# Kernel tuning notes

Measured on AMD Instinct MI355X. Metric: run time of the kernel, lower is better.

The kernel has to match this reference:

```python
import jax, jax.numpy as jnp
import numpy as np

INPUTS = 41024  # halfkp feature count (64 king squares * 641)
L1, L2, L3 = 128, 32, 32
B = 4096
ACTIVE_P = 30.0 / INPUTS  # ~30 active features per position


def setup_inputs() -> dict:
    key = jax.random.key(0)
    ks = jax.random.split(key, 10)
    # side-to-move indicators: us in {0,1}, them = 1 - us
    us = jax.random.randint(ks[0], (B, 1), 0, 2).astype(jnp.float32)
    them = 1.0 - us
    # sparse halfkp feature vectors (~30 active one-hot features per row)
    def sparse_feats(k):
        k1, k2 = jax.random.split(k)
        mask = jax.random.bernoulli(k1, ACTIVE_P, (B, INPUTS))
        return mask.astype(jnp.float32)
    w_in = sparse_feats(ks[1])
    b_in = sparse_feats(ks[2])
    s = 0.02
    W_ft = jax.random.normal(ks[3], (INPUTS, L1), dtype=jnp.float32) * s
    b_ft = jax.random.normal(ks[4], (L1,), dtype=jnp.float32) * s
    W1 = jax.random.normal(ks[5], (2 * L1, L2), dtype=jnp.float32) * s
    b1 = jax.random.normal(ks[6], (L2,), dtype=jnp.float32) * s
    W2 = jax.random.normal(ks[7], (L2, L3), dtype=jnp.float32) * s
    b2 = jax.random.normal(ks[8], (L3,), dtype=jnp.float32) * s
    Wo = jax.random.normal(ks[9], (L3, 1), dtype=jnp.float32) * s
    bo = jnp.zeros((1,), dtype=jnp.float32)
    return {"us": us, "them": them, "w_in": w_in, "b_in": b_in,
            "W_ft": W_ft, "b_ft": b_ft, "W1": W1, "b1": b1,
            "W2": W2, "b2": b2, "Wo": Wo, "bo": bo}


def reference(us, them, w_in, b_in, W_ft, b_ft, W1, b1, W2, b2, Wo, bo):
    # feature transformer (shared weights for white/black perspectives)
    w = w_in @ W_ft + b_ft  # [B, L1]
    b = b_in @ W_ft + b_ft  # [B, L1]
    l0 = us * jnp.concatenate([w, b], axis=1) + them * jnp.concatenate([b, w], axis=1)
    l0 = jnp.clip(l0, 0.0, 1.0)
    l1 = jnp.clip(l0 @ W1 + b1, 0.0, 1.0)
    l2 = jnp.clip(l1 @ W2 + b2, 0.0, 1.0)
    return l2 @ Wo + bo  # [B, 1]
```

## Files before the change

### kernel.cpp

```cpp
#include <hip/hip_runtime.h>
#include <hip/hip_bf16.h>

#define NNUE_INPUTS 41024
#define L1N 128
#define L2N 32
#define L3N 32
#define MAX_ACT 512

__device__ __forceinline__ float clip01(float x) {
    return fminf(fmaxf(x, 0.0f), 1.0f);
}

__global__ __launch_bounds__(256, 4) void nnue_fused_kernel(
    const float* __restrict__ us, const float* __restrict__ them,
    const float* __restrict__ w_in, const float* __restrict__ b_in,
    const float* __restrict__ W_ft, const float* __restrict__ b_ft,
    const float* __restrict__ W1, const float* __restrict__ b1,
    const float* __restrict__ W2, const float* __restrict__ b2,
    const float* __restrict__ Wo, const float* __restrict__ bo,
    float* __restrict__ out)
{
    __shared__ int   s_idx_w[MAX_ACT];
    __shared__ int   s_idx_b[MAX_ACT];
    __shared__ int   s_cnt[2];
    __shared__ float s_w[L1N];
    __shared__ float s_b[L1N];
    __shared__ float s_l0[2 * L1N];
    __shared__ float s_part[8][L2N];
    __shared__ float s_l1[L2N];
    __shared__ float s_l2[L3N];

    const int row = blockIdx.x;
    const int tid = threadIdx.x;

    if (tid < 2) s_cnt[tid] = 0;
    const float u = us[row];
    const float t = them[row];
    __syncthreads();

    const float4* wr = (const float4*)(w_in + (size_t)row * NNUE_INPUTS);
    const float4* br = (const float4*)(b_in + (size_t)row * NNUE_INPUTS);
    const int nv8 = NNUE_INPUTS / 8;

    for (int v = tid; v < nv8; v += 256) {
        const float4 a0 = wr[2 * v];
        const float4 a1 = wr[2 * v + 1];
        const float4 c0 = br[2 * v];
        const float4 c1 = br[2 * v + 1];
        const float sw = ((a0.x + a0.y) + (a0.z + a0.w)) + ((a1.x + a1.y) + (a1.z + a1.w));
        const float sb = ((c0.x + c0.y) + (c0.z + c0.w)) + ((c1.x + c1.y) + (c1.z + c1.w));
        if (__any((sw != 0.0f) || (sb != 0.0f))) {
            const int base = v * 8;
            if (sw != 0.0f) {
                unsigned m = (a0.x != 0.0f ?   1u : 0u) | (a0.y != 0.0f ?   2u : 0u)
                           | (a0.z != 0.0f ?   4u : 0u) | (a0.w != 0.0f ?   8u : 0u)
                           | (a1.x != 0.0f ?  16u : 0u) | (a1.y != 0.0f ?  32u : 0u)
                           | (a1.z != 0.0f ?  64u : 0u) | (a1.w != 0.0f ? 128u : 0u);
                while (m) {
                    const int b = __ffs(m) - 1; m &= m - 1;
                    const int p = atomicAdd(&s_cnt[0], 1);
                    s_idx_w[p & (MAX_ACT - 1)] = base + b;
                }
            }
            if (sb != 0.0f) {
                unsigned m = (c0.x != 0.0f ?   1u : 0u) | (c0.y != 0.0f ?   2u : 0u)
                           | (c0.z != 0.0f ?   4u : 0u) | (c0.w != 0.0f ?   8u : 0u)
                           | (c1.x != 0.0f ?  16u : 0u) | (c1.y != 0.0f ?  32u : 0u)
                           | (c1.z != 0.0f ?  64u : 0u) | (c1.w != 0.0f ? 128u : 0u);
                while (m) {
                    const int b = __ffs(m) - 1; m &= m - 1;
                    const int p = atomicAdd(&s_cnt[1], 1);
                    s_idx_b[p & (MAX_ACT - 1)] = base + b;
                }
            }
        }
    }
    __syncthreads();

    const int kw = min(s_cnt[0], MAX_ACT);
    const int kb = min(s_cnt[1], MAX_ACT);

    {
        const int  c    = tid & (L1N - 1);
        const bool is_b = tid >= L1N;
        const int* lst  = is_b ? s_idx_b : s_idx_w;
        const int  K    = is_b ? kb : kw;
        const float* Wc = W_ft + c;
        float acc = b_ft[c];
        int k = 0;
        for (; k + 4 <= K; k += 4) {
            const int i0 = lst[k], i1 = lst[k + 1], i2 = lst[k + 2], i3 = lst[k + 3];
            const float f0 = Wc[(size_t)i0 * L1N];
            const float f1 = Wc[(size_t)i1 * L1N];
            const float f2 = Wc[(size_t)i2 * L1N];
            const float f3 = Wc[(size_t)i3 * L1N];
            acc += f0; acc += f1; acc += f2; acc += f3;
        }
        for (; k < K; ++k) acc += Wc[(size_t)lst[k] * L1N];
        if (is_b) s_b[c] = acc; else s_w[c] = acc;
    }
    __syncthreads();

    if (tid < L1N) {
        const float wv = s_w[tid], bv = s_b[tid];
        s_l0[tid]       = clip01(u * wv + t * bv);
        s_l0[L1N + tid] = clip01(u * bv + t * wv);
    }
    __syncthreads();

    {
        const int o  = tid & 31;
        const int ch = tid >> 5;
        float a = 0.0f;
        const int k0 = ch * 32;
        #pragma unroll
        for (int k = 0; k < 32; ++k) {
            a += s_l0[k0 + k] * W1[(k0 + k) * L2N + o];
        }
        s_part[ch][o] = a;
    }
    __syncthreads();
    if (tid < L2N) {
        float a = b1[tid];
        #pragma unroll
        for (int j = 0; j < 8; ++j) a += s_part[j][tid];
        s_l1[tid] = clip01(a);
    }
    __syncthreads();

    if (tid < L3N) {
        float a = b2[tid];
        #pragma unroll
        for (int k = 0; k < L2N; ++k) a += s_l1[k] * W2[k * L3N + tid];
        s_l2[tid] = clip01(a);
    }
    __syncthreads();

    if (tid == 0) {
        float a = bo[0];
        #pragma unroll
        for (int k = 0; k < L3N; ++k) a += s_l2[k] * Wo[k];
        out[row] = a;
    }
}

extern "C" void kernel_launch(void* const* d_in, const int* in_sizes, int n_in,
                              void* d_out, int out_size, void* d_ws, size_t ws_size,
                              hipStream_t stream) {
    const float* us   = (const float*)d_in[0];
    const float* them = (const float*)d_in[1];
    const float* w_in = (const float*)d_in[2];
    const float* b_in = (const float*)d_in[3];
    const float* W_ft = (const float*)d_in[4];
    const float* b_ft = (const float*)d_in[5];
    const float* W1   = (const float*)d_in[6];
    const float* b1   = (const float*)d_in[7];
    const float* W2   = (const float*)d_in[8];
    const float* b2   = (const float*)d_in[9];
    const float* Wo   = (const float*)d_in[10];
    const float* bo   = (const float*)d_in[11];
    float* out = (float*)d_out;

    const int B = in_sizes[0];
    nnue_fused_kernel<<<dim3(B), dim3(256), 0, stream>>>(
        us, them, w_in, b_in, W_ft, b_ft, W1, b1, W2, b2, Wo, bo, out);
}
```

Baseline: 1.234 ms.

## Split sparse-input scan into a separate grid-strided kernel with global index lists

The per-row nonzero scan of the dense one-hot inputs moves into its own kernel. That kernel uses a fixed 2048-block grid that streams both input matrices flat with four independent float4 loads per iteration, and it appends active feature indices to per-row lists in workspace using global atomics. A second kernel reads those lists and does the feature-transformer gather and the small MLP. The goal is better memory-level parallelism and bandwidth on the dominant 1.3 GB streaming read. The cost is a memset, an extra launch, global atomic traffic, and index lists that are no longer in order, which changes the float summation order.

```diff
diff --git a/kernel.cpp b/kernel.cpp
--- a/kernel.cpp
+++ b/kernel.cpp
@@ -2,6 +2,7 @@
 #include <hip/hip_bf16.h>
 
 #define NNUE_INPUTS 41024
+#define NV4_ROW (NNUE_INPUTS / 4)
 #define L1N 128
 #define L2N 32
 #define L3N 32
@@ -11,18 +12,69 @@
     return fminf(fmaxf(x, 0.0f), 1.0f);
 }
 
-__global__ __launch_bounds__(256, 4) void nnue_fused_kernel(
+__global__ __launch_bounds__(256, 8) void nnue_scan_kernel(
+    const float* __restrict__ w_in, const float* __restrict__ b_in,
+    int* __restrict__ cnt,
+    int* __restrict__ idx,
+    int rows)
+{
+    const int  half = gridDim.x >> 1;
+    const int  p    = (blockIdx.x >= half) ? 1 : 0;
+    const int  blk  = p ? (blockIdx.x - half) : blockIdx.x;
+    const float4* src = (const float4*)(p ? b_in : w_in);
+    int* mycnt = cnt + (size_t)p * rows;
+    int* myidx = idx + (size_t)p * rows * MAX_ACT;
+
+    const long NV4    = (long)rows * NV4_ROW;
+    const long tcount = (long)half * 256;
+
+    auto put = [&](int e) {
+        const int r  = (unsigned)e / NNUE_INPUTS;
+        const int f  = e - r * NNUE_INPUTS;
+        const int pp = atomicAdd(&mycnt[r], 1);
+        myidx[(size_t)r * MAX_ACT + (pp & (MAX_ACT - 1))] = f;
+    };
+    auto emit = [&](const float4& x, long v) {
+        const float s = (x.x + x.y) + (x.z + x.w);
+        if (s != 0.0f) {
+            const int e = (int)(v * 4);
+            if (x.x != 0.0f) put(e);
+            if (x.y != 0.0f) put(e + 1);
+            if (x.z != 0.0f) put(e + 2);
+            if (x.w != 0.0f) put(e + 3);
+        }
+    };
+
+    long v = (long)blk * 256 + threadIdx.x;
+    for (; v + 3 * tcount < NV4; v += 4 * tcount) {
+        const float4 x0 = src[v];
+        const float4 x1 = src[v + tcount];
+        const float4 x2 = src[v + 2 * tcount];
+        const float4 x3 = src[v + 3 * tcount];
+        const float s = (((x0.x + x0.y) + (x0.z + x0.w)) + ((x1.x + x1.y) + (x1.z + x1.w)))
+                      + (((x2.x + x2.y) + (x2.z + x2.w)) + ((x3.x + x3.y) + (x3.z + x3.w)));
+        if (__any(s != 0.0f)) {
+            emit(x0, v);
+            emit(x1, v + tcount);
+            emit(x2, v + 2 * tcount);
+            emit(x3, v + 3 * tcount);
+        }
+    }
+    for (; v < NV4; v += tcount) {
+        const float4 x = src[v];
+        emit(x, v);
+    }
+}
+
+__global__ __launch_bounds__(256, 8) void nnue_tail_kernel(
     const float* __restrict__ us, const float* __restrict__ them,
-    const float* __restrict__ w_in, const float* __restrict__ b_in,
     const float* __restrict__ W_ft, const float* __restrict__ b_ft,
     const float* __restrict__ W1, const float* __restrict__ b1,
     const float* __restrict__ W2, const float* __restrict__ b2,
     const float* __restrict__ Wo, const float* __restrict__ bo,
-    float* __restrict__ out)
+    const int* __restrict__ cnt, const int* __restrict__ idx,
+    float* __restrict__ out, int rows)
 {
-    __shared__ int   s_idx_w[MAX_ACT];
-    __shared__ int   s_idx_b[MAX_ACT];
-    __shared__ int   s_cnt[2];
     __shared__ float s_w[L1N];
     __shared__ float s_b[L1N];
     __shared__ float s_l0[2 * L1N];
@@ -32,59 +84,14 @@
 
     const int row = blockIdx.x;
     const int tid = threadIdx.x;
-
-    if (tid < 2) s_cnt[tid] = 0;
     const float u = us[row];
     const float t = them[row];
-    __syncthreads();
-
-    const float4* wr = (const float4*)(w_in + (size_t)row * NNUE_INPUTS);
-    const float4* br = (const float4*)(b_in + (size_t)row * NNUE_INPUTS);
-    const int nv8 = NNUE_INPUTS / 8;
-
-    for (int v = tid; v < nv8; v += 256) {
-        const float4 a0 = wr[2 * v];
-        const float4 a1 = wr[2 * v + 1];
-        const float4 c0 = br[2 * v];
-        const float4 c1 = br[2 * v + 1];
-        const float sw = ((a0.x + a0.y) + (a0.z + a0.w)) + ((a1.x + a1.y) + (a1.z + a1.w));
-        const float sb = ((c0.x + c0.y) + (c0.z + c0.w)) + ((c1.x + c1.y) + (c1.z + c1.w));
-        if (__any((sw != 0.0f) || (sb != 0.0f))) {
-            const int base = v * 8;
-            if (sw != 0.0f) {
-                unsigned m = (a0.x != 0.0f ?   1u : 0u) | (a0.y != 0.0f ?   2u : 0u)
-                           | (a0.z != 0.0f ?   4u : 0u) | (a0.w != 0.0f ?   8u : 0u)
-                           | (a1.x != 0.0f ?  16u : 0u) | (a1.y != 0.0f ?  32u : 0u)
-                           | (a1.z != 0.0f ?  64u : 0u) | (a1.w != 0.0f ? 128u : 0u);
-                while (m) {
-                    const int b = __ffs(m) - 1; m &= m - 1;
-                    const int p = atomicAdd(&s_cnt[0], 1);
-                    s_idx_w[p & (MAX_ACT - 1)] = base + b;
-                }
-            }
-            if (sb != 0.0f) {
-                unsigned m = (c0.x != 0.0f ?   1u : 0u) | (c0.y != 0.0f ?   2u : 0u)
-                           | (c0.z != 0.0f ?   4u : 0u) | (c0.w != 0.0f ?   8u : 0u)
-                           | (c1.x != 0.0f ?  16u : 0u) | (c1.y != 0.0f ?  32u : 0u)
-                           | (c1.z != 0.0f ?  64u : 0u) | (c1.w != 0.0f ? 128u : 0u);
-                while (m) {
-                    const int b = __ffs(m) - 1; m &= m - 1;
-                    const int p = atomicAdd(&s_cnt[1], 1);
-                    s_idx_b[p & (MAX_ACT - 1)] = base + b;
-                }
-            }
-        }
-    }
-    __syncthreads();
-
-    const int kw = min(s_cnt[0], MAX_ACT);
-    const int kb = min(s_cnt[1], MAX_ACT);
 
     {
         const int  c    = tid & (L1N - 1);
-        const bool is_b = tid >= L1N;
-        const int* lst  = is_b ? s_idx_b : s_idx_w;
-        const int  K    = is_b ? kb : kw;
+        const int  p    = (tid >= L1N) ? 1 : 0;
+        const int  K    = min(cnt[(size_t)p * rows + row], MAX_ACT);
+        const int* lst  = idx + ((size_t)p * rows + row) * MAX_ACT;
         const float* Wc = W_ft + c;
         float acc = b_ft[c];
         int k = 0;
@@ -97,7 +104,7 @@
             acc += f0; acc += f1; acc += f2; acc += f3;
         }
         for (; k < K; ++k) acc += Wc[(size_t)lst[k] * L1N];
-        if (is_b) s_b[c] = acc; else s_w[c] = acc;
+        if (p) s_b[c] = acc; else s_w[c] = acc;
     }
     __syncthreads();
 
@@ -114,9 +121,7 @@
         float a = 0.0f;
         const int k0 = ch * 32;
         #pragma unroll
-        for (int k = 0; k < 32; ++k) {
-            a += s_l0[k0 + k] * W1[(k0 + k) * L2N + o];
-        }
+        for (int k = 0; k < 32; ++k) a += s_l0[k0 + k] * W1[(k0 + k) * L2N + o];
         s_part[ch][o] = a;
     }
     __syncthreads();
@@ -161,7 +166,15 @@
     const float* bo   = (const float*)d_in[11];
     float* out = (float*)d_out;
 
-    const int B = in_sizes[0];
-    nnue_fused_kernel<<<dim3(B), dim3(256), 0, stream>>>(
-        us, them, w_in, b_in, W_ft, b_ft, W1, b1, W2, b2, Wo, bo, out);
+    const int rows = in_sizes[0];
+
+    int* cnt = (int*)d_ws;
+    int* idx = cnt + 2 * (size_t)rows;
+
+    hipMemsetAsync(cnt, 0, 2 * (size_t)rows * sizeof(int), stream);
+
+    nnue_scan_kernel<<<dim3(2048), dim3(256), 0, stream>>>(w_in, b_in, cnt, idx, rows);
+
+    nnue_tail_kernel<<<dim3(rows), dim3(256), 0, stream>>>(
+        us, them, W_ft, b_ft, W1, b1, W2, b2, Wo, bo, cnt, idx, out, rows);
 }
```

Result: slower. 1.302 ms (+5.6%).

## Split feature scan per wave and software-prefetch next float4 batch

Applied to the files above, without the earlier changes.

Restructures the sparse-feature scan so that each wave owns one half of either the white or the black input row, instead of every thread reading both rows. Each lane now loads four strided float4s per iteration and issues the next iteration's loads before processing the current ones, which keeps more memory requests in flight. The goal is to hide global load latency in a scan that is dominated by streaming memory reads. The trade-off is higher register use for the prefetch buffers, plus a small tail path for the leftover float4s.

```diff
diff --git a/kernel.cpp b/kernel.cpp
--- a/kernel.cpp
+++ b/kernel.cpp
@@ -6,6 +6,11 @@
 #define L2N 32
 #define L3N 32
 #define MAX_ACT 512
+#define NC_ROW (NNUE_INPUTS / 4)
+#define NC_HALF (NC_ROW / 2)
+#define WITER 20
+
+typedef float f4 __attribute__((ext_vector_type(4)));
 
 __device__ __forceinline__ float clip01(float x) {
     return fminf(fmaxf(x, 0.0f), 1.0f);
@@ -30,49 +35,57 @@
     __shared__ float s_l1[L2N];
     __shared__ float s_l2[L3N];
 
-    const int row = blockIdx.x;
-    const int tid = threadIdx.x;
+    const int row  = blockIdx.x;
+    const int tid  = threadIdx.x;
+    const int wave = tid >> 6;
+    const int lane = tid & 63;
 
     if (tid < 2) s_cnt[tid] = 0;
     const float u = us[row];
     const float t = them[row];
     __syncthreads();
 
-    const float4* wr = (const float4*)(w_in + (size_t)row * NNUE_INPUTS);
-    const float4* br = (const float4*)(b_in + (size_t)row * NNUE_INPUTS);
-    const int nv8 = NNUE_INPUTS / 8;
+    {
+        const int     p    = wave >> 1;
+        const f4*     src  = (const f4*)((p ? b_in : w_in) + (size_t)row * NNUE_INPUTS);
+        int*          mcnt = &s_cnt[p];
+        int*          midx = p ? s_idx_b : s_idx_w;
+        const int     base = (wave & 1) * NC_HALF;
 
-    for (int v = tid; v < nv8; v += 256) {
-        const float4 a0 = wr[2 * v];
-        const float4 a1 = wr[2 * v + 1];
-        const float4 c0 = br[2 * v];
-        const float4 c1 = br[2 * v + 1];
-        const float sw = ((a0.x + a0.y) + (a0.z + a0.w)) + ((a1.x + a1.y) + (a1.z + a1.w));
-        const float sb = ((c0.x + c0.y) + (c0.z + c0.w)) + ((c1.x + c1.y) + (c1.z + c1.w));
-        if (__any((sw != 0.0f) || (sb != 0.0f))) {
-            const int base = v * 8;
-            if (sw != 0.0f) {
-                unsigned m = (a0.x != 0.0f ?   1u : 0u) | (a0.y != 0.0f ?   2u : 0u)
-                           | (a0.z != 0.0f ?   4u : 0u) | (a0.w != 0.0f ?   8u : 0u)
-                           | (a1.x != 0.0f ?  16u : 0u) | (a1.y != 0.0f ?  32u : 0u)
-                           | (a1.z != 0.0f ?  64u : 0u) | (a1.w != 0.0f ? 128u : 0u);
-                while (m) {
-                    const int b = __ffs(m) - 1; m &= m - 1;
-                    const int p = atomicAdd(&s_cnt[0], 1);
-                    s_idx_w[p & (MAX_ACT - 1)] = base + b;
-                }
+        auto emit = [&](const f4& x, int c) {
+            const int e = c * 4;
+            if (x[0] != 0.0f) { int q = atomicAdd(mcnt, 1); midx[q & (MAX_ACT - 1)] = e;     }
+            if (x[1] != 0.0f) { int q = atomicAdd(mcnt, 1); midx[q & (MAX_ACT - 1)] = e + 1; }
+            if (x[2] != 0.0f) { int q = atomicAdd(mcnt, 1); midx[q & (MAX_ACT - 1)] = e + 2; }
+            if (x[3] != 0.0f) { int q = atomicAdd(mcnt, 1); midx[q & (MAX_ACT - 1)] = e + 3; }
+        };
+        auto proc4 = [&](int c0, const f4& x0, const f4& x1, const f4& x2, const f4& x3) {
+            const float s = (((x0[0] + x0[1]) + (x0[2] + x0[3])) + ((x1[0] + x1[1]) + (x1[2] + x1[3])))
+                          + (((x2[0] + x2[1]) + (x2[2] + x2[3])) + ((x3[0] + x3[1]) + (x3[2] + x3[3])));
+            if (__any(s != 0.0f)) {
+                emit(x0, c0);
+                emit(x1, c0 + 64);
+                emit(x2, c0 + 128);
+                emit(x3, c0 + 192);
             }
-            if (sb != 0.0f) {
-                unsigned m = (c0.x != 0.0f ?   1u : 0u) | (c0.y != 0.0f ?   2u : 0u)
-                           | (c0.z != 0.0f ?   4u : 0u) | (c0.w != 0.0f ?   8u : 0u)
-                           | (c1.x != 0.0f ?  16u : 0u) | (c1.y != 0.0f ?  32u : 0u)
-                           | (c1.z != 0.0f ?  64u : 0u) | (c1.w != 0.0f ? 128u : 0u);
-                while (m) {
-                    const int b = __ffs(m) - 1; m &= m - 1;
-                    const int p = atomicAdd(&s_cnt[1], 1);
-                    s_idx_b[p & (MAX_ACT - 1)] = base + b;
-                }
-            }
+        };
+
+        int c = base + lane;
+        f4 x0 = src[c], x1 = src[c + 64], x2 = src[c + 128], x3 = src[c + 192];
+        #pragma unroll 1
+        for (int i = 0; i < WITER - 1; ++i) {
+            const int cn = c + 256;
+            const f4 n0 = src[cn], n1 = src[cn + 64], n2 = src[cn + 128], n3 = src[cn + 192];
+            proc4(c, x0, x1, x2, x3);
+            x0 = n0; x1 = n1; x2 = n2; x3 = n3;
+            c = cn;
+        }
+        proc4(c, x0, x1, x2, x3);
+        if (lane < NC_HALF - WITER * 256) {
+            const int ct = base + WITER * 256 + lane;
+            const f4 x = src[ct];
+            const float s = (x[0] + x[1]) + (x[2] + x[3]);
+            if (__any(s != 0.0f)) { if (s != 0.0f) emit(x, ct); }
         }
     }
     __syncthreads();
@@ -81,12 +94,12 @@
     const int kb = min(s_cnt[1], MAX_ACT);
 
     {
-        const int  c    = tid & (L1N - 1);
+        const int  ch   = tid & (L1N - 1);
         const bool is_b = tid >= L1N;
         const int* lst  = is_b ? s_idx_b : s_idx_w;
         const int  K    = is_b ? kb : kw;
-        const float* Wc = W_ft + c;
-        float acc = b_ft[c];
+        const float* Wc = W_ft + ch;
+        float acc = b_ft[ch];
         int k = 0;
         for (; k + 4 <= K; k += 4) {
             const int i0 = lst[k], i1 = lst[k + 1], i2 = lst[k + 2], i3 = lst[k + 3];
@@ -97,7 +110,7 @@
             acc += f0; acc += f1; acc += f2; acc += f3;
         }
         for (; k < K; ++k) acc += Wc[(size_t)lst[k] * L1N];
-        if (is_b) s_b[c] = acc; else s_w[c] = acc;
+        if (is_b) s_b[ch] = acc; else s_w[ch] = acc;
     }
     __syncthreads();
 
@@ -114,9 +127,7 @@
         float a = 0.0f;
         const int k0 = ch * 32;
         #pragma unroll
-        for (int k = 0; k < 32; ++k) {
-            a += s_l0[k0 + k] * W1[(k0 + k) * L2N + o];
-        }
+        for (int k = 0; k < 32; ++k) a += s_l0[k0 + k] * W1[(k0 + k) * L2N + o];
         s_part[ch][o] = a;
     }
     __syncthreads();
```

Result: no change. 1.227 ms (median of 2 runs) (-0.5%).
